# Kernel tuning notes

Measured on AMD Instinct MI355X. Metric: run time of the kernel, lower is better.

## Reference

```python
import math
import jax, jax.numpy as jnp
import numpy as np

# ---- Clifford algebra Cl(1,3) tables (static, built in numpy) ----
DIM = 4
METRIC = np.array([1.0, -1.0, -1.0, -1.0], dtype=np.float64)
N_COMP = 1 << DIM  # 16 multivector components
SUBSPACES = np.array([math.comb(DIM, g) for g in range(DIM + 1)])  # [1,4,6,4,1]

def _popcount(x):
    return bin(x).count("1")

# blades ordered by (grade, bitmask) as in CGENN-style algebras
_BLADES = sorted(range(N_COMP), key=lambda b: (_popcount(b), b))
_IDX = {b: i for i, b in enumerate(_BLADES)}

def _blade_prod(a, b):
    # canonical reordering sign
    s, t = 0, a >> 1
    while t:
        s += _popcount(t & b)
        t >>= 1
    sign = -1.0 if (s % 2) else 1.0
    for i in range(DIM):
        if (a >> i) & 1 and (b >> i) & 1:
            sign *= METRIC[i]
    return a ^ b, sign

# cayley[i, j, k]: coefficient of e_j in e_i * e_k  (matches einsum '...i,ijk,...k->...j')
CAYLEY = np.zeros((N_COMP, N_COMP, N_COMP), dtype=np.float32)
for a in range(N_COMP):
    for b in range(N_COMP):
        c, s = _blade_prod(a, b)
        CAYLEY[_IDX[a], _IDX[c], _IDX[b]] = s

GRADES = np.array([_popcount(b) for b in _BLADES])
BETA = np.array([float(np.prod([METRIC[i] for i in range(DIM) if (b >> i) & 1])) for b in _BLADES], dtype=np.float32)  # blade quadratic-form signs
GRADE_ONEHOT = (GRADES[:, None] == np.arange(DIM + 1)[None, :]).astype(np.float32)  # [16,5]

_sl = np.concatenate([[0], np.cumsum(SUBSPACES)])
PATHS = np.zeros((DIM + 1,) * 3, dtype=bool)
for i in range(DIM + 1):
    for j in range(DIM + 1):
        for k in range(DIM + 1):
            PATHS[i, j, k] = np.any(CAYLEY[_sl[i]:_sl[i+1], _sl[j]:_sl[j+1], _sl[k]:_sl[k+1]] != 0)
PI, PJ, PK = np.nonzero(PATHS)
N_PATHS = int(PATHS.sum())  # 35 for Cl(1,3)
EPS = 1e-6


def mvlinear(x, w):
    # x: [b, m, 16], w: [n, m, 5] (one scalar weight per grade) -> [b, n, 16]
    w16 = jnp.repeat(w, SUBSPACES, axis=-1)  # [n, m, 16]
    return jnp.einsum('bmi,nmi->bni', x, w16)


def normalize(x, a):
    # per-grade norm: |b(x_g, x_g)|^0.5, gated by sigmoid(a)
    q = ((x * x) * BETA) @ GRADE_ONEHOT            # [b, n, 5]
    norms = jnp.sqrt(jnp.abs(q))
    norms = jax.nn.sigmoid(a) * (norms - 1.0) + 1.0
    norms16 = jnp.repeat(norms, SUBSPACES, axis=-1)  # [b, n, 16]
    return x / (norms16 + EPS)


def get_weight(gp_weight):
    # scatter [F, 35] params into [F,5,5,5], expand to [F,16,16,16], mask by Cayley
    F = gp_weight.shape[0]
    w = jnp.zeros((F, DIM + 1, DIM + 1, DIM + 1), gp_weight.dtype).at[:, PI, PJ, PK].set(gp_weight)
    w = jnp.repeat(w, SUBSPACES, axis=1)
    w = jnp.repeat(w, SUBSPACES, axis=2)
    w = jnp.repeat(w, SUBSPACES, axis=3)
    return jnp.asarray(CAYLEY) * w  # [F,16,16,16]


def setup_inputs() -> dict:
    key = jax.random.key(0)
    k0, k1, k2, k3, k4 = jax.random.split(key, 5)
    B, F = 4096, 512
    x = jax.random.normal(k0, (B, F, N_COMP), jnp.float32)
    s = 1.0 / math.sqrt(F)
    w_left = jax.random.normal(k1, (F, F, DIM + 1), jnp.float32) * s
    b_left = jax.random.normal(k2, (F,), jnp.float32) * 0.01
    w_right = jax.random.normal(k3, (F, F, DIM + 1), jnp.float32) * s
    a_norm = jnp.zeros((F, DIM + 1), jnp.float32)  # normalization_init = 0
    gp_weight = jax.random.normal(k4, (F, N_PATHS), jnp.float32) * (1.0 / math.sqrt(DIM + 1))
    return {"x": x, "w_left": w_left, "b_left": b_left, "w_right": w_right,
            "a_norm": a_norm, "gp_weight": gp_weight}


def reference(x, w_left, b_left, w_right, a_norm, gp_weight):
    input_right = normalize(mvlinear(x, w_right), a_norm)
    W = get_weight(gp_weight)                       # [F,16,16,16]
    gp = jnp.einsum('bni,nijk,bnk->bnj', x, W, input_right)
    left = mvlinear(x, w_left).at[..., 0].add(b_left)  # bias embedded at grade-0 component
    return (left + gp) / math.sqrt(2.0)
```

## Files before the change

kernel.cpp:

```cpp
#include <hip/hip_runtime.h>

typedef unsigned int uint;
typedef unsigned short ushort;
typedef __attribute__((ext_vector_type(8))) short bf16x8;
typedef __attribute__((ext_vector_type(4))) float f32x4;

struct GPTables {
    signed char jid[16][16];
    float       sgn[16][16];
    signed char pid[16][16];
    float       beta[16];
    signed char grade[16];
};

constexpr int popc4(int x) { return ((x >> 0) & 1) + ((x >> 1) & 1) + ((x >> 2) & 1) + ((x >> 3) & 1); }

constexpr GPTables make_tables() {
    GPTables T{};
    int blades[16] = {0, 1, 2, 4, 8, 3, 5, 6, 9, 10, 12, 7, 11, 13, 14, 15};
    int idxof[16] = {};
    for (int i = 0; i < 16; ++i) idxof[blades[i]] = i;
    float metric[4] = {1.f, -1.f, -1.f, -1.f};
    for (int i = 0; i < 16; ++i) {
        T.grade[i] = (signed char)popc4(blades[i]);
        float b = 1.f;
        for (int bit = 0; bit < 4; ++bit)
            if ((blades[i] >> bit) & 1) b *= metric[bit];
        T.beta[i] = b;
    }
    bool paths[5][5][5] = {};
    for (int a = 0; a < 16; ++a)
        for (int b = 0; b < 16; ++b)
            paths[popc4(a)][popc4(a ^ b)][popc4(b)] = true;
    int pid3[5][5][5] = {};
    int cnt = 0;
    for (int gi = 0; gi < 5; ++gi)
        for (int gj = 0; gj < 5; ++gj)
            for (int gk = 0; gk < 5; ++gk)
                if (paths[gi][gj][gk]) pid3[gi][gj][gk] = cnt++;
    for (int ii = 0; ii < 16; ++ii) {
        for (int kk = 0; kk < 16; ++kk) {
            int a = blades[ii], b = blades[kk];
            int c = a ^ b;
            int s = 0, t = a >> 1;
            while (t) { s += popc4(t & b); t >>= 1; }
            float sign = (s & 1) ? -1.f : 1.f;
            for (int bit = 0; bit < 4; ++bit)
                if (((a >> bit) & 1) && ((b >> bit) & 1)) sign *= metric[bit];
            T.jid[ii][kk] = (signed char)idxof[c];
            T.sgn[ii][kk] = sign;
            T.pid[ii][kk] = (signed char)pid3[popc4(a)][popc4(c)][popc4(b)];
        }
    }
    return T;
}

constexpr GPTables TBL = make_tables();
__constant__ signed char GRADE_OF_C[16] = {0, 1, 1, 1, 1, 2, 2, 2, 2, 2, 2, 3, 3, 3, 3, 4};

#define BF (4096)
#define FF (512)
#define BM_ (2097152)

__device__ inline ushort f2bf(float f) {
    uint u = __float_as_uint(f);
    uint r = (u + 0x7fffu + ((u >> 16) & 1u)) >> 16;
    return (ushort)r;
}
__device__ inline float bf2f(ushort h) { return __uint_as_float(((uint)h) << 16); }

__global__ __launch_bounds__(256) void k_transpose_x(const float* __restrict__ x,
                                                     ushort* __restrict__ Xh,
                                                     ushort* __restrict__ Xl) {
    const int p0 = (blockIdx.x * 256 + threadIdx.x) * 2;
    float v[32];
    const float4* x4 = (const float4*)(x + (size_t)p0 * 16);
#pragma unroll
    for (int j = 0; j < 8; ++j) {
        float4 t = x4[j];
        v[j * 4 + 0] = t.x; v[j * 4 + 1] = t.y; v[j * 4 + 2] = t.z; v[j * 4 + 3] = t.w;
    }
#pragma unroll
    for (int i = 0; i < 16; ++i) {
        ushort h0 = f2bf(v[i]),      h1 = f2bf(v[16 + i]);
        ushort l0 = f2bf(v[i] - bf2f(h0));
        ushort l1 = f2bf(v[16 + i] - bf2f(h1));
        *(uint*)&Xh[(size_t)i * BM_ + p0] = (uint)h0 | ((uint)h1 << 16);
        *(uint*)&Xl[(size_t)i * BM_ + p0] = (uint)l0 | ((uint)l1 << 16);
    }
}

__global__ __launch_bounds__(256) void k_prep_w(const float* __restrict__ w_right,
                                                const float* __restrict__ w_left,
                                                ushort* __restrict__ Wb) {
    const int n = blockIdx.x;
    const int m = threadIdx.x * 2;
#pragma unroll
    for (int g = 0; g < 5; ++g) {
        float a = w_right[(size_t)n * (FF * 5) + (size_t)m * 5 + g];
        float b = w_right[(size_t)n * (FF * 5) + (size_t)(m + 1) * 5 + g];
        ushort ah = f2bf(a), bh = f2bf(b);
        ushort al = f2bf(a - bf2f(ah)), bl = f2bf(b - bf2f(bh));
        *(uint*)&Wb[(size_t)g * (FF * FF) + (size_t)n * FF + m] = (uint)ah | ((uint)bh << 16);
        *(uint*)&Wb[(size_t)(5 + g) * (FF * FF) + (size_t)n * FF + m] = (uint)al | ((uint)bl << 16);
        float c = w_left[(size_t)n * (FF * 5) + (size_t)m * 5 + g];
        float d = w_left[(size_t)n * (FF * 5) + (size_t)(m + 1) * 5 + g];
        *(uint*)&Wb[(size_t)(10 + g) * (FF * FF) + (size_t)n * FF + m] =
            (uint)f2bf(c) | ((uint)f2bf(d) << 16);
    }
}

__global__ __launch_bounds__(256) void k_gemm_right(const ushort* __restrict__ Xh,
                                                    const ushort* __restrict__ Xl,
                                                    const ushort* __restrict__ Wb,
                                                    float* __restrict__ OutR) {
    const int comp = blockIdx.z;
    const ushort* Ah = Xh + (size_t)comp * BM_;
    const ushort* Al = Xl + (size_t)comp * BM_;
    const int g = GRADE_OF_C[comp];
    const ushort* Bh = Wb + (size_t)g * (FF * FF);
    const ushort* Bl = Wb + (size_t)(5 + g) * (FF * FF);
    float* C = OutR + (size_t)comp * BM_;
    const int m0 = blockIdx.x * 128;
    const int n0 = blockIdx.y * 128;

    __shared__ ushort Ahs[128][32], Als[128][32], Bhs[128][32], Bls[128][32];

    const int tid = threadIdx.x;
    const int lane = tid & 63, wid = tid >> 6;
    const int wm = wid >> 1, wn = wid & 1;
    const int lr = lane & 15, lk = (lane >> 4) * 8;

    f32x4 acc[4][4] = {};

    for (int k0 = 0; k0 < FF; k0 += 32) {
#pragma unroll
        for (int pass = 0; pass < 2; ++pass) {
            int q = tid + pass * 256;
            int row = q >> 2;
            int col = (q & 3) * 8;
            *(uint4*)&Ahs[row][col] = *(const uint4*)&Ah[(size_t)(m0 + row) * FF + k0 + col];
            *(uint4*)&Als[row][col] = *(const uint4*)&Al[(size_t)(m0 + row) * FF + k0 + col];
            *(uint4*)&Bhs[row][col] = *(const uint4*)&Bh[(size_t)(n0 + row) * FF + k0 + col];
            *(uint4*)&Bls[row][col] = *(const uint4*)&Bl[(size_t)(n0 + row) * FF + k0 + col];
        }
        __syncthreads();
        bf16x8 ah[4], al[4], bh[4], bl[4];
#pragma unroll
        for (int mb = 0; mb < 4; ++mb) {
            ah[mb] = *(const bf16x8*)&Ahs[wm * 64 + mb * 16 + lr][lk];
            al[mb] = *(const bf16x8*)&Als[wm * 64 + mb * 16 + lr][lk];
        }
#pragma unroll
        for (int nb = 0; nb < 4; ++nb) {
            bh[nb] = *(const bf16x8*)&Bhs[wn * 64 + nb * 16 + lr][lk];
            bl[nb] = *(const bf16x8*)&Bls[wn * 64 + nb * 16 + lr][lk];
        }
#pragma unroll
        for (int mb = 0; mb < 4; ++mb)
#pragma unroll
            for (int nb = 0; nb < 4; ++nb) {
                acc[mb][nb] = __builtin_amdgcn_mfma_f32_16x16x32_bf16(ah[mb], bh[nb], acc[mb][nb], 0, 0, 0);
                acc[mb][nb] = __builtin_amdgcn_mfma_f32_16x16x32_bf16(ah[mb], bl[nb], acc[mb][nb], 0, 0, 0);
                acc[mb][nb] = __builtin_amdgcn_mfma_f32_16x16x32_bf16(al[mb], bh[nb], acc[mb][nb], 0, 0, 0);
            }
        __syncthreads();
    }

#pragma unroll
    for (int mb = 0; mb < 4; ++mb)
#pragma unroll
        for (int nb = 0; nb < 4; ++nb) {
            int row = m0 + wm * 64 + mb * 16 + (lane >> 4) * 4;
            int col = n0 + wn * 64 + nb * 16 + (lane & 15);
#pragma unroll
            for (int r = 0; r < 4; ++r)
                C[(size_t)(row + r) * FF + col] = acc[mb][nb][r];
        }
}

__global__ __launch_bounds__(256) void k_gemm_left(const ushort* __restrict__ Xh,
                                                   const ushort* __restrict__ Wb,
                                                   ushort* __restrict__ OutL) {
    const int comp = blockIdx.z;
    const ushort* A = Xh + (size_t)comp * BM_;
    const ushort* Bw = Wb + (size_t)(10 + GRADE_OF_C[comp]) * (FF * FF);
    ushort* C = OutL + (size_t)comp * BM_;
    const int m0 = blockIdx.x * 128;
    const int n0 = blockIdx.y * 128;

    __shared__ ushort As[128][32], Bs[128][32];

    const int tid = threadIdx.x;
    const int lane = tid & 63, wid = tid >> 6;
    const int wm = wid >> 1, wn = wid & 1;
    const int lr = lane & 15, lk = (lane >> 4) * 8;

    f32x4 acc[4][4] = {};

    for (int k0 = 0; k0 < FF; k0 += 32) {
#pragma unroll
        for (int pass = 0; pass < 2; ++pass) {
            int q = tid + pass * 256;
            int row = q >> 2;
            int col = (q & 3) * 8;
            *(uint4*)&As[row][col] = *(const uint4*)&A[(size_t)(m0 + row) * FF + k0 + col];
            *(uint4*)&Bs[row][col] = *(const uint4*)&Bw[(size_t)(n0 + row) * FF + k0 + col];
        }
        __syncthreads();
        bf16x8 af[4], bfr[4];
#pragma unroll
        for (int mb = 0; mb < 4; ++mb) af[mb] = *(const bf16x8*)&As[wm * 64 + mb * 16 + lr][lk];
#pragma unroll
        for (int nb = 0; nb < 4; ++nb) bfr[nb] = *(const bf16x8*)&Bs[wn * 64 + nb * 16 + lr][lk];
#pragma unroll
        for (int mb = 0; mb < 4; ++mb)
#pragma unroll
            for (int nb = 0; nb < 4; ++nb)
                acc[mb][nb] = __builtin_amdgcn_mfma_f32_16x16x32_bf16(af[mb], bfr[nb], acc[mb][nb], 0, 0, 0);
        __syncthreads();
    }

#pragma unroll
    for (int mb = 0; mb < 4; ++mb)
#pragma unroll
        for (int nb = 0; nb < 4; ++nb) {
            int row = m0 + wm * 64 + mb * 16 + (lane >> 4) * 4;
            int col = n0 + wn * 64 + nb * 16 + (lane & 15);
#pragma unroll
            for (int r = 0; r < 4; ++r)
                C[(size_t)(row + r) * FF + col] = f2bf(acc[mb][nb][r]);
        }
}

__global__ __launch_bounds__(256) void k_gp(const float* __restrict__ x,
                                            const float* __restrict__ OutR,
                                            const ushort* __restrict__ OutL,
                                            const float* __restrict__ gpw,
                                            const float* __restrict__ a_norm,
                                            const float* __restrict__ b_left,
                                            float* __restrict__ out) {
    const int bn = blockIdx.x * 256 + threadIdx.x;
    const int n = bn & (FF - 1);

    float xi[16];
    {
        const float4* xp = (const float4*)(x + (size_t)bn * 16);
#pragma unroll
        for (int j = 0; j < 4; ++j) {
            float4 t = xp[j];
            xi[j * 4 + 0] = t.x; xi[j * 4 + 1] = t.y; xi[j * 4 + 2] = t.z; xi[j * 4 + 3] = t.w;
        }
    }

    float R[16];
#pragma unroll
    for (int i = 0; i < 16; ++i) R[i] = OutR[(size_t)i * BM_ + bn];

    float q[5] = {0.f, 0.f, 0.f, 0.f, 0.f};
#pragma unroll
    for (int i = 0; i < 16; ++i) q[TBL.grade[i]] += TBL.beta[i] * R[i] * R[i];
    float inv[5];
#pragma unroll
    for (int g = 0; g < 5; ++g) {
        float nr = sqrtf(fabsf(q[g]));
        float a = a_norm[(size_t)n * 5 + g];
        float sig = 1.f / (1.f + __expf(-a));
        float nf = sig * (nr - 1.f) + 1.f + 1e-6f;
        inv[g] = 1.f / nf;
    }
#pragma unroll
    for (int i = 0; i < 16; ++i) R[i] *= inv[TBL.grade[i]];

    float pw[35];
#pragma unroll
    for (int p = 0; p < 35; ++p) pw[p] = gpw[(size_t)n * 35 + p];

    float acc[16] = {};
#pragma unroll
    for (int ii = 0; ii < 16; ++ii) {
#pragma unroll
        for (int kk = 0; kk < 16; ++kk) {
            const int j = TBL.jid[ii][kk];
            const int p = TBL.pid[ii][kk];
            const float s = TBL.sgn[ii][kk];
            acc[j] += (s * pw[p]) * (xi[ii] * R[kk]);
        }
    }

    const float bl = b_left[n];
    float o[16];
#pragma unroll
    for (int j = 0; j < 16; ++j) {
        float l = bf2f(OutL[(size_t)j * BM_ + bn]);
        if (j == 0) l += bl;
        o[j] = (l + acc[j]) * 0.70710678118654752440f;
    }
    float4* op = (float4*)(out + (size_t)bn * 16);
#pragma unroll
    for (int j = 0; j < 4; ++j) {
        float4 t;
        t.x = o[j * 4 + 0]; t.y = o[j * 4 + 1]; t.z = o[j * 4 + 2]; t.w = o[j * 4 + 3];
        op[j] = t;
    }
}

extern "C" void kernel_launch(void* const* d_in, const int* in_sizes, int n_in,
                              void* d_out, int out_size, void* d_ws, size_t ws_size,
                              hipStream_t stream) {
    (void)in_sizes; (void)n_in; (void)out_size; (void)ws_size;
    const float* x       = (const float*)d_in[0];
    const float* w_left  = (const float*)d_in[1];
    const float* b_left  = (const float*)d_in[2];
    const float* w_right = (const float*)d_in[3];
    const float* a_norm  = (const float*)d_in[4];
    const float* gpw     = (const float*)d_in[5];
    float* out = (float*)d_out;

    char* ws = (char*)d_ws;
    ushort* Xh   = (ushort*)ws;
    ushort* Xl   = (ushort*)(ws + 67108864);
    ushort* Wb   = (ushort*)(ws + 134217728);
    float*  OutR = (float*)(ws + 142082048);
    ushort* OutL = (ushort*)(ws + 276299776);

    k_transpose_x<<<4096, 256, 0, stream>>>(x, Xh, Xl);
    k_prep_w<<<512, 256, 0, stream>>>(w_right, w_left, Wb);
    dim3 g(32, 4, 16);
    k_gemm_right<<<g, 256, 0, stream>>>(Xh, Xl, Wb, OutR);
    k_gemm_left<<<g, 256, 0, stream>>>(Xh, Wb, OutL);
    k_gp<<<8192, 256, 0, stream>>>(x, OutR, OutL, gpw, a_norm, b_left, out);
}
```

Before: 406.1 us.

## Fuse left and right GEMMs, use direct-to-LDS swizzled loads, stage gp params in LDS

Merges the separate right (split-bf16, 3 MFMA) and left (1 MFMA) GEMM kernels into one kernel so the Xh tile is loaded once for both. Tile loads now go global-to-LDS directly, with an XOR swizzle on the LDS layout to reduce bank conflicts. Launch bounds request 2 blocks per SM. The gp kernel stages per-feature weights, norm params and bias in shared memory with coalesced loads. The trade-off is more accumulator registers (two 4x4 accumulator sets) and more LDS per block, which may limit occupancy.

```diff
diff --git a/kernel.cpp b/kernel.cpp
--- a/kernel.cpp
+++ b/kernel.cpp
@@ -56,11 +56,11 @@
 }
 
 constexpr GPTables TBL = make_tables();
-__constant__ signed char GRADE_OF_C[16] = {0, 1, 1, 1, 1, 2, 2, 2, 2, 2, 2, 3, 3, 3, 3, 4};
 
 #define BF (4096)
 #define FF (512)
 #define BM_ (2097152)
+#define FFFF (262144)
 
 __device__ inline ushort f2bf(float f) {
     uint u = __float_as_uint(f);
@@ -68,6 +68,12 @@
     return (ushort)r;
 }
 __device__ inline float bf2f(ushort h) { return __uint_as_float(((uint)h) << 16); }
+
+typedef __attribute__((address_space(3))) uint lds_u32;
+typedef const __attribute__((address_space(1))) uint g_u32;
+__device__ __forceinline__ void gload16(const void* gsrc, void* ldst) {
+    __builtin_amdgcn_global_load_lds((g_u32*)gsrc, (lds_u32*)ldst, 16, 0, 0);
+}
 
 __global__ __launch_bounds__(256) void k_transpose_x(const float* __restrict__ x,
                                                      ushort* __restrict__ Xh,
@@ -101,72 +107,92 @@
         float b = w_right[(size_t)n * (FF * 5) + (size_t)(m + 1) * 5 + g];
         ushort ah = f2bf(a), bh = f2bf(b);
         ushort al = f2bf(a - bf2f(ah)), bl = f2bf(b - bf2f(bh));
-        *(uint*)&Wb[(size_t)g * (FF * FF) + (size_t)n * FF + m] = (uint)ah | ((uint)bh << 16);
-        *(uint*)&Wb[(size_t)(5 + g) * (FF * FF) + (size_t)n * FF + m] = (uint)al | ((uint)bl << 16);
+        *(uint*)&Wb[(size_t)g * FFFF + (size_t)n * FF + m] = (uint)ah | ((uint)bh << 16);
+        *(uint*)&Wb[(size_t)(5 + g) * FFFF + (size_t)n * FF + m] = (uint)al | ((uint)bl << 16);
         float c = w_left[(size_t)n * (FF * 5) + (size_t)m * 5 + g];
         float d = w_left[(size_t)n * (FF * 5) + (size_t)(m + 1) * 5 + g];
-        *(uint*)&Wb[(size_t)(10 + g) * (FF * FF) + (size_t)n * FF + m] =
+        *(uint*)&Wb[(size_t)(10 + g) * FFFF + (size_t)n * FF + m] =
             (uint)f2bf(c) | ((uint)f2bf(d) << 16);
     }
 }
 
-__global__ __launch_bounds__(256) void k_gemm_right(const ushort* __restrict__ Xh,
-                                                    const ushort* __restrict__ Xl,
-                                                    const ushort* __restrict__ Wb,
-                                                    float* __restrict__ OutR) {
+__device__ __forceinline__ bf16x8 ldfrag(const ushort* tile, int row, int colb) {
+    return *(const bf16x8*)((const char*)tile + row * 64 + (colb ^ ((row & 3) << 4)));
+}
+
+__global__ __launch_bounds__(256, 2) void k_gemm(const ushort* __restrict__ Xh,
+                                                 const ushort* __restrict__ Xl,
+                                                 const ushort* __restrict__ Wb,
+                                                 float* __restrict__ OutR,
+                                                 ushort* __restrict__ OutL) {
     const int comp = blockIdx.z;
+    const int g = TBL.grade[comp];
     const ushort* Ah = Xh + (size_t)comp * BM_;
     const ushort* Al = Xl + (size_t)comp * BM_;
-    const int g = GRADE_OF_C[comp];
-    const ushort* Bh = Wb + (size_t)g * (FF * FF);
-    const ushort* Bl = Wb + (size_t)(5 + g) * (FF * FF);
-    float* C = OutR + (size_t)comp * BM_;
+    const ushort* Bh = Wb + (size_t)g * FFFF;
+    const ushort* Bl = Wb + (size_t)(5 + g) * FFFF;
+    const ushort* BL = Wb + (size_t)(10 + g) * FFFF;
     const int m0 = blockIdx.x * 128;
     const int n0 = blockIdx.y * 128;
 
-    __shared__ ushort Ahs[128][32], Als[128][32], Bhs[128][32], Bls[128][32];
+    __shared__ ushort sh[5 * 128 * 32];
+    ushort* tA  = sh;
+    ushort* tAl = sh + 1 * 4096;
+    ushort* tBh = sh + 2 * 4096;
+    ushort* tBl = sh + 3 * 4096;
+    ushort* tBL = sh + 4 * 4096;
 
     const int tid = threadIdx.x;
     const int lane = tid & 63, wid = tid >> 6;
     const int wm = wid >> 1, wn = wid & 1;
-    const int lr = lane & 15, lk = (lane >> 4) * 8;
-
-    f32x4 acc[4][4] = {};
+    const int lr = lane & 15;
+    const int kb = (lane >> 4) * 16;
+
+    f32x4 accR[4][4] = {};
+    f32x4 accL[4][4] = {};
 
     for (int k0 = 0; k0 < FF; k0 += 32) {
 #pragma unroll
         for (int pass = 0; pass < 2; ++pass) {
-            int q = tid + pass * 256;
-            int row = q >> 2;
-            int col = (q & 3) * 8;
-            *(uint4*)&Ahs[row][col] = *(const uint4*)&Ah[(size_t)(m0 + row) * FF + k0 + col];
-            *(uint4*)&Als[row][col] = *(const uint4*)&Al[(size_t)(m0 + row) * FF + k0 + col];
-            *(uint4*)&Bhs[row][col] = *(const uint4*)&Bh[(size_t)(n0 + row) * FF + k0 + col];
-            *(uint4*)&Bls[row][col] = *(const uint4*)&Bl[(size_t)(n0 + row) * FF + k0 + col];
+            const int c = tid + pass * 256;
+            const int row = c >> 2;
+            const int scb = ((c & 3) * 16) ^ ((row & 3) << 4);
+            const size_t gb = (size_t)row * (FF * 2) + (size_t)k0 * 2 + scb;
+            const size_t mb_ = (size_t)m0 * (FF * 2), nb_ = (size_t)n0 * (FF * 2);
+            char* dst = (char*)sh + c * 16;
+            gload16((const char*)Ah + mb_ + gb, dst);
+            gload16((const char*)Al + mb_ + gb, dst + 8192);
+            gload16((const char*)Bh + nb_ + gb, dst + 16384);
+            gload16((const char*)Bl + nb_ + gb, dst + 24576);
+            gload16((const char*)BL + nb_ + gb, dst + 32768);
         }
         __syncthreads();
-        bf16x8 ah[4], al[4], bh[4], bl[4];
+        bf16x8 ah[4], al[4], bh[4], bl[4], bLf[4];
 #pragma unroll
         for (int mb = 0; mb < 4; ++mb) {
-            ah[mb] = *(const bf16x8*)&Ahs[wm * 64 + mb * 16 + lr][lk];
-            al[mb] = *(const bf16x8*)&Als[wm * 64 + mb * 16 + lr][lk];
+            ah[mb] = ldfrag(tA,  wm * 64 + mb * 16 + lr, kb);
+            al[mb] = ldfrag(tAl, wm * 64 + mb * 16 + lr, kb);
         }
 #pragma unroll
         for (int nb = 0; nb < 4; ++nb) {
-            bh[nb] = *(const bf16x8*)&Bhs[wn * 64 + nb * 16 + lr][lk];
-            bl[nb] = *(const bf16x8*)&Bls[wn * 64 + nb * 16 + lr][lk];
+            bh[nb]  = ldfrag(tBh, wn * 64 + nb * 16 + lr, kb);
+            bl[nb]  = ldfrag(tBl, wn * 64 + nb * 16 + lr, kb);
+            bLf[nb] = ldfrag(tBL, wn * 64 + nb * 16 + lr, kb);
         }
 #pragma unroll
         for (int mb = 0; mb < 4; ++mb)
 #pragma unroll
             for (int nb = 0; nb < 4; ++nb) {
-                acc[mb][nb] = __builtin_amdgcn_mfma_f32_16x16x32_bf16(ah[mb], bh[nb], acc[mb][nb], 0, 0, 0);
-                acc[mb][nb] = __builtin_amdgcn_mfma_f32_16x16x32_bf16(ah[mb], bl[nb], acc[mb][nb], 0, 0, 0);
-                acc[mb][nb] = __builtin_amdgcn_mfma_f32_16x16x32_bf16(al[mb], bh[nb], acc[mb][nb], 0, 0, 0);
+                accR[mb][nb] = __builtin_amdgcn_mfma_f32_16x16x32_bf16(ah[mb], bh[nb],  accR[mb][nb], 0, 0, 0);
+                accR[mb][nb] = __builtin_amdgcn_mfma_f32_16x16x32_bf16(ah[mb], bl[nb],  accR[mb][nb], 0, 0, 0);
+                accR[mb][nb] = __builtin_amdgcn_mfma_f32_16x16x32_bf16(al[mb], bh[nb],  accR[mb][nb], 0, 0, 0);
+                accL[mb][nb] = __builtin_amdgcn_mfma_f32_16x16x32_bf16(ah[mb], bLf[nb], accL[mb][nb], 0, 0, 0);
             }
         __syncthreads();
     }
 
+    float* CR = OutR + (size_t)comp * BM_;
+    ushort* CL = OutL + (size_t)comp * BM_;
 #pragma unroll
     for (int mb = 0; mb < 4; ++mb)
 #pragma unroll
@@ -174,62 +200,10 @@
             int row = m0 + wm * 64 + mb * 16 + (lane >> 4) * 4;
             int col = n0 + wn * 64 + nb * 16 + (lane & 15);
 #pragma unroll
-            for (int r = 0; r < 4; ++r)
-                C[(size_t)(row + r) * FF + col] = acc[mb][nb][r];
-        }
-}
-
-__global__ __launch_bounds__(256) void k_gemm_left(const ushort* __restrict__ Xh,
-                                                   const ushort* __restrict__ Wb,
-                                                   ushort* __restrict__ OutL) {
-    const int comp = blockIdx.z;
-    const ushort* A = Xh + (size_t)comp * BM_;
-    const ushort* Bw = Wb + (size_t)(10 + GRADE_OF_C[comp]) * (FF * FF);
-    ushort* C = OutL + (size_t)comp * BM_;
-    const int m0 = blockIdx.x * 128;
-    const int n0 = blockIdx.y * 128;
-
-    __shared__ ushort As[128][32], Bs[128][32];
-
-    const int tid = threadIdx.x;
-    const int lane = tid & 63, wid = tid >> 6;
-    const int wm = wid >> 1, wn = wid & 1;
-    const int lr = lane & 15, lk = (lane >> 4) * 8;
-
-    f32x4 acc[4][4] = {};
-
-    for (int k0 = 0; k0 < FF; k0 += 32) {
-#pragma unroll
-        for (int pass = 0; pass < 2; ++pass) {
-            int q = tid + pass * 256;
-            int row = q >> 2;
-            int col = (q & 3) * 8;
-            *(uint4*)&As[row][col] = *(const uint4*)&A[(size_t)(m0 + row) * FF + k0 + col];
-            *(uint4*)&Bs[row][col] = *(const uint4*)&Bw[(size_t)(n0 + row) * FF + k0 + col];
-        }
-        __syncthreads();
-        bf16x8 af[4], bfr[4];
-#pragma unroll
-        for (int mb = 0; mb < 4; ++mb) af[mb] = *(const bf16x8*)&As[wm * 64 + mb * 16 + lr][lk];
-#pragma unroll
-        for (int nb = 0; nb < 4; ++nb) bfr[nb] = *(const bf16x8*)&Bs[wn * 64 + nb * 16 + lr][lk];
-#pragma unroll
-        for (int mb = 0; mb < 4; ++mb)
-#pragma unroll
-            for (int nb = 0; nb < 4; ++nb)
-                acc[mb][nb] = __builtin_amdgcn_mfma_f32_16x16x32_bf16(af[mb], bfr[nb], acc[mb][nb], 0, 0, 0);
-        __syncthreads();
-    }
-
-#pragma unroll
-    for (int mb = 0; mb < 4; ++mb)
-#pragma unroll
-        for (int nb = 0; nb < 4; ++nb) {
-            int row = m0 + wm * 64 + mb * 16 + (lane >> 4) * 4;
-            int col = n0 + wn * 64 + nb * 16 + (lane & 15);
-#pragma unroll
-            for (int r = 0; r < 4; ++r)
-                C[(size_t)(row + r) * FF + col] = f2bf(acc[mb][nb][r]);
+            for (int r = 0; r < 4; ++r) {
+                CR[(size_t)(row + r) * FF + col] = accR[mb][nb][r];
+                CL[(size_t)(row + r) * FF + col] = f2bf(accL[mb][nb][r]);
+            }
         }
 }
 
@@ -240,8 +214,19 @@
                                             const float* __restrict__ a_norm,
                                             const float* __restrict__ b_left,
                                             float* __restrict__ out) {
-    const int bn = blockIdx.x * 256 + threadIdx.x;
-    const int n = bn & (FF - 1);
+    __shared__ float s_pw[256 * 35];
+    __shared__ float s_an[256 * 5];
+    __shared__ float s_bl[256];
+
+    const int tid = threadIdx.x;
+    const int bn = blockIdx.x * 256 + tid;
+    const int n0 = (blockIdx.x & 1) * 256;
+
+    for (int i = tid; i < 256 * 35; i += 256) s_pw[i] = gpw[(size_t)n0 * 35 + i];
+#pragma unroll
+    for (int i = 0; i < 5; ++i) s_an[tid + i * 256] = a_norm[(size_t)n0 * 5 + tid + i * 256];
+    s_bl[tid] = b_left[n0 + tid];
+    __syncthreads();
 
     float xi[16];
     {
@@ -264,7 +249,7 @@
 #pragma unroll
     for (int g = 0; g < 5; ++g) {
         float nr = sqrtf(fabsf(q[g]));
-        float a = a_norm[(size_t)n * 5 + g];
+        float a = s_an[tid * 5 + g];
         float sig = 1.f / (1.f + __expf(-a));
         float nf = sig * (nr - 1.f) + 1.f + 1e-6f;
         inv[g] = 1.f / nf;
@@ -274,7 +259,7 @@
 
     float pw[35];
 #pragma unroll
-    for (int p = 0; p < 35; ++p) pw[p] = gpw[(size_t)n * 35 + p];
+    for (int p = 0; p < 35; ++p) pw[p] = s_pw[tid * 35 + p];
 
     float acc[16] = {};
 #pragma unroll
@@ -288,7 +273,7 @@
         }
     }
 
-    const float bl = b_left[n];
+    const float bl = s_bl[tid];
     float o[16];
 #pragma unroll
     for (int j = 0; j < 16; ++j) {
@@ -327,7 +312,6 @@
     k_transpose_x<<<4096, 256, 0, stream>>>(x, Xh, Xl);
     k_prep_w<<<512, 256, 0, stream>>>(w_right, w_left, Wb);
     dim3 g(32, 4, 16);
-    k_gemm_right<<<g, 256, 0, stream>>>(Xh, Xl, Wb, OutR);
-    k_gemm_left<<<g, 256, 0, stream>>>(Xh, Wb, OutL);
+    k_gemm<<<g, 256, 0, stream>>>(Xh, Xl, Wb, OutR, OutL);
     k_gp<<<8192, 256, 0, stream>>>(x, OutR, OutL, gpw, a_norm, b_left, out);
 }
```

Measured after the change: 367.4 us. -9.5%, faster.
